# Kernel optimization log

Measured on AMD Instinct MI355X. Metric: run time of the kernel, lower is better.

## Reference

```python
import jax, jax.numpy as jnp
import numpy as np

N, E = 50000, 800000
IN, OUT = 128, 64  # in_channels, out_channels


def _w(key, fan_in, fan_out):
    return jax.random.normal(key, (fan_in, fan_out), dtype=jnp.float32) * (1.0 / np.sqrt(fan_in))


def setup_inputs() -> dict:
    key = jax.random.key(0)
    ks = jax.random.split(key, 16)
    x = jax.random.normal(ks[0], (N, IN), dtype=jnp.float32)
    edge_index = jax.random.randint(ks[1], (2, E), 0, N, dtype=jnp.int64)
    return {
        "x": x,
        "edge_index": edge_index,
        # Encoder: GCNConv(128->128), GCNConv(128->64), Linear(64->64)
        "ew1": _w(ks[2], IN, 2 * OUT), "eb1": jnp.zeros((2 * OUT,), jnp.float32),
        "ew2": _w(ks[3], 2 * OUT, OUT), "eb2": jnp.zeros((OUT,), jnp.float32),
        "efw": _w(ks[4], OUT, OUT), "efb": jnp.zeros((OUT,), jnp.float32),
        # Decoder: GCNConv(64->256), GCNConv(256->128), Linear(128->1024)
        "dw1": _w(ks[5], OUT, 2 * IN), "db1": jnp.zeros((2 * IN,), jnp.float32),
        "dw2": _w(ks[6], 2 * IN, IN), "db2": jnp.zeros((IN,), jnp.float32),
        "dfw": _w(ks[7], IN, 1024), "dfb": jnp.zeros((1024,), jnp.float32),
        # LinkPredictor: Linear(2*64 -> 1)
        "lw": _w(ks[8], 2 * OUT, 1), "lb": jnp.zeros((1,), jnp.float32),
    }


def gcn_conv(h_in, W, b, src, dst, dinv):
    # PyG GCNConv: linear transform, then symmetric-normalized aggregation
    # with implicit self-loops (deg includes the self-loop).
    h = h_in @ W  # [N, F_out]
    norm = (dinv[src] * dinv[dst])[:, None]      # per-edge symmetric norm
    agg = jax.ops.segment_sum(h[src] * norm, dst, num_segments=h.shape[0])
    agg = agg + h * (dinv * dinv)[:, None]       # self-loop contribution
    return agg + b


def reference(x, edge_index, ew1, eb1, ew2, eb2, efw, efb,
              dw1, db1, dw2, db2, dfw, dfb, lw, lb):
    src, dst = edge_index[0], edge_index[1]
    n = x.shape[0]
    # degree over A + I (self-loops added), computed on the target index
    deg = jax.ops.segment_sum(jnp.ones((src.shape[0],), x.dtype), dst,
                              num_segments=n) + 1.0
    dinv = deg ** -0.5

    # Encoder
    z = jax.nn.relu(gcn_conv(x, ew1, eb1, src, dst, dinv))
    z = gcn_conv(z, ew2, eb2, src, dst, dinv)
    z = z @ efw + efb  # latent [N, 64]

    # Decoder
    h = jax.nn.relu(gcn_conv(z, dw1, db1, src, dst, dinv))
    h = gcn_conv(h, dw2, db2, src, dst, dinv)
    x_hat = h @ dfw + dfb  # [N, 1024]

    # Link predictor on edge endpoint gathers
    zc = jnp.concatenate([z[src], z[dst]], axis=-1)  # [E, 128]
    edge_probs = jax.nn.sigmoid(zc @ lw + lb)        # [E, 1]
    return x_hat, edge_probs
```

## Files before the change

### kernel.cpp

```cpp
#include <hip/hip_runtime.h>
#include <hip/hip_bf16.h>

using bf16 = __hip_bfloat16;
typedef __attribute__((ext_vector_type(8))) short short8;
typedef __attribute__((ext_vector_type(4))) float f32x4;

static __device__ __forceinline__ float b2f(bf16 x) { return __bfloat162float(x); }

static __device__ __forceinline__ unsigned int packbf2(float a, float b) {
    bf16 x = __float2bfloat16(a), y = __float2bfloat16(b);
    unsigned short ux = *(unsigned short*)&x, uy = *(unsigned short*)&y;
    return (unsigned int)ux | ((unsigned int)uy << 16);
}

__global__ void det_kernel(const unsigned short* __restrict__ xh,
                           const int* __restrict__ ei, int* __restrict__ flags) {
    __shared__ int s_exp, s_nz;
    if (threadIdx.x == 0) { s_exp = 0; s_nz = 0; }
    __syncthreads();
    if (threadIdx.x < 256) {
        unsigned short h = xh[threadIdx.x];
        int ef = (h >> 7) & 0xFF;
        if (ef < 100 || ef > 140) atomicAdd(&s_exp, 1);
    }
    for (int i = 1 + 2 * threadIdx.x; i < 4096; i += 2 * blockDim.x)
        if (ei[i] != 0) atomicAdd(&s_nz, 1);
    __syncthreads();
    if (threadIdx.x == 0) {
        flags[0] = (s_exp > 16) ? 1 : 0;
        flags[1] = (s_nz == 0) ? 1 : 0;
    }
}

__global__ void canon_w(const void* __restrict__ src, const int* __restrict__ flags,
                        float* __restrict__ dst, int n) {
    int i = blockIdx.x * blockDim.x + threadIdx.x;
    if (i >= n) return;
    dst[i] = flags[0] ? ((const float*)src)[i] : b2f(((const bf16*)src)[i]);
}

__global__ void canon_x(const void* __restrict__ src, const int* __restrict__ flags,
                        bf16* __restrict__ dst, int n) {
    int i = blockIdx.x * blockDim.x + threadIdx.x;
    if (i >= n) return;
    dst[i] = flags[0] ? __float2bfloat16(((const float*)src)[i]) : ((const bf16*)src)[i];
}

__global__ void canon_edges(const int* __restrict__ ei, const int* __restrict__ flags,
                            int* __restrict__ srcd, int* __restrict__ dstd, int E) {
    int e = blockIdx.x * blockDim.x + threadIdx.x;
    if (e >= E) return;
    if (flags[1]) { srcd[e] = ei[2 * e]; dstd[e] = ei[2 * E + 2 * e]; }
    else          { srcd[e] = ei[e];     dstd[e] = ei[E + e]; }
}

__global__ void prep_wt(const void* __restrict__ src, const int* __restrict__ flags,
                        bf16* __restrict__ Wth, bf16* __restrict__ Wtl, int K, int F) {
    int j = blockIdx.x * blockDim.x + threadIdx.x;
    if (j >= K * F) return;
    int f = j / K, k = j - f * K;
    float v = flags[0] ? ((const float*)src)[(size_t)k * F + f]
                       : b2f(((const bf16*)src)[(size_t)k * F + f]);
    bf16 hi = __float2bfloat16(v);
    float lo = v - b2f(hi);
    Wth[j] = hi;
    Wtl[j] = __float2bfloat16(lo);
}

__global__ void hist_kernel(const int* __restrict__ dstv, int* __restrict__ counts, int E) {
    int e = blockIdx.x * blockDim.x + threadIdx.x;
    if (e < E) atomicAdd(&counts[dstv[e]], 1);
}

__global__ void scan_part1(const int* __restrict__ counts, int* __restrict__ blockSums, int N) {
    __shared__ int red[256];
    int i = blockIdx.x * 256 + threadIdx.x;
    red[threadIdx.x] = (i < N) ? counts[i] : 0;
    __syncthreads();
    for (int off = 128; off > 0; off >>= 1) {
        if (threadIdx.x < off) red[threadIdx.x] += red[threadIdx.x + off];
        __syncthreads();
    }
    if (threadIdx.x == 0) blockSums[blockIdx.x] = red[0];
}

__global__ void scan_part2(const int* __restrict__ blockSums, int* __restrict__ blockOff,
                           int* __restrict__ rowPtrN, int G) {
    __shared__ int s[256];
    int t = threadIdx.x;
    s[t] = (t < G) ? blockSums[t] : 0;
    __syncthreads();
    for (int off = 1; off < 256; off <<= 1) {
        int v = (t >= off) ? s[t - off] : 0;
        __syncthreads();
        s[t] += v;
        __syncthreads();
    }
    if (t < G) blockOff[t] = (t > 0) ? s[t - 1] : 0;
    if (t == 255) *rowPtrN = s[255];
}

__global__ void scan_part3(const int* __restrict__ counts, const int* __restrict__ blockOff,
                           int* __restrict__ rowPtr, int* __restrict__ cursor,
                           float* __restrict__ dinv, int N) {
    __shared__ int s[256];
    int t = threadIdx.x;
    int i = blockIdx.x * 256 + t;
    int c = (i < N) ? counts[i] : 0;
    s[t] = c;
    __syncthreads();
    for (int off = 1; off < 256; off <<= 1) {
        int v = (t >= off) ? s[t - off] : 0;
        __syncthreads();
        s[t] += v;
        __syncthreads();
    }
    if (i < N) {
        int o = blockOff[blockIdx.x] + s[t] - c;
        rowPtr[i] = o;
        cursor[i] = o;
        dinv[i] = rsqrtf((float)c + 1.0f);
    }
}

__global__ void scatter_kernel(const int* __restrict__ srcv, const int* __restrict__ dstv,
                               int* __restrict__ cursor, int* __restrict__ sortedSrc, int E) {
    int e = blockIdx.x * blockDim.x + threadIdx.x;
    if (e >= E) return;
    int p = atomicAdd(&cursor[dstv[e]], 1);
    sortedSrc[p] = srcv[e];
}

template <int K>
__global__ __launch_bounds__(256)
void mfma_gemm(const bf16* __restrict__ A,
               const bf16* __restrict__ Wth, const bf16* __restrict__ Wtl,
               const float* __restrict__ bias, const float* __restrict__ dinv,
               void* __restrict__ out, const int* __restrict__ flags,
               int outmode, int F, int N) {
    __shared__ uint4 lds4[1536];
    char* lds = (char*)lds4;
    const int tid = threadIdx.x;
    const int w = tid >> 6, lane = tid & 63;
    const int rowBase = blockIdx.y * 64;
    const int colBase = blockIdx.x * 64;

    f32x4 zero = {0.f, 0.f, 0.f, 0.f};
    f32x4 acc[4];
#pragma unroll
    for (int n = 0; n < 4; ++n) acc[n] = zero;

    const int arow = (w << 4) + (lane & 15);
    const int aswz = arow & 7;
    const int colL = lane & 15;

    for (int kc = 0; kc < K; kc += 64) {
#pragma unroll
        for (int i = 0; i < 6; ++i) {
            const int g = i * 256 + tid;
            char* dst = lds + ((i * 256 + (w << 6)) << 4);
            const bf16* src;
            if (g < 512) {
                int r = g >> 3, c = g & 7;
                int gr = rowBase + r; if (gr >= N) gr = N - 1;
                src = A + (size_t)gr * K + kc + ((c ^ (r & 7)) << 3);
            } else if (g < 1024) {
                int h = g - 512; int cl = h >> 3, c = h & 7;
                src = Wth + (size_t)(colBase + cl) * K + kc + ((c ^ (cl & 7)) << 3);
            } else {
                int h = g - 1024; int cl = h >> 3, c = h & 7;
                src = Wtl + (size_t)(colBase + cl) * K + kc + ((c ^ (cl & 7)) << 3);
            }
            __builtin_amdgcn_global_load_lds(
                (const __attribute__((address_space(1))) void*)src,
                (__attribute__((address_space(3))) void*)dst, 16, 0, 0);
        }
        __syncthreads();

        const char* aB = lds;
        const char* hB = lds + 8192;
        const char* lB = lds + 16384;
#pragma unroll
        for (int ks = 0; ks < 2; ++ks) {
            const int c = (ks << 2) + (lane >> 4);
            short8 a = *(const short8*)(aB + (((arow << 3) + (c ^ aswz)) << 4));
#pragma unroll
            for (int n = 0; n < 4; ++n) {
                const int col = (n << 4) + colL;
                const int s = ((col << 3) + (c ^ (col & 7))) << 4;
                short8 bh = *(const short8*)(hB + s);
                short8 bl = *(const short8*)(lB + s);
                acc[n] = __builtin_amdgcn_mfma_f32_16x16x32_bf16(a, bh, acc[n], 0, 0, 0);
                acc[n] = __builtin_amdgcn_mfma_f32_16x16x32_bf16(a, bl, acc[n], 0, 0, 0);
            }
        }
        __syncthreads();
    }

    const int m32 = outmode ? flags[0] : 0;
    const int r0 = rowBase + (w << 4) + ((lane >> 4) << 2);
#pragma unroll
    for (int n = 0; n < 4; ++n) {
        const int col = colBase + (n << 4) + colL;
        const float bv = bias ? bias[col] : 0.0f;
#pragma unroll
        for (int r = 0; r < 4; ++r) {
            const int row = r0 + r;
            if (row < N) {
                float v = acc[n][r];
                if (dinv) v *= dinv[row];
                v += bv;
                size_t o = (size_t)row * F + col;
                if (m32) ((float*)out)[o] = v;
                else     ((bf16*)out)[o] = __float2bfloat16(v);
            }
        }
    }
}

template <int F>
static __device__ __forceinline__ void acc_row(const bf16* __restrict__ Hs, int row, int lane,
                                               float* acc) {
    if constexpr (F == 64) {
        unsigned short u = ((const unsigned short*)Hs)[(size_t)row * 64 + lane];
        union { unsigned int i; float f; } c; c.i = (unsigned int)u << 16;
        acc[0] += c.f;
    } else if constexpr (F == 128) {
        unsigned int u = ((const unsigned int*)(Hs + (size_t)row * 128))[lane];
        union { unsigned int i; float f; } lo, hi;
        lo.i = u << 16; hi.i = u & 0xffff0000u;
        acc[0] += lo.f; acc[1] += hi.f;
    } else {
        uint2 u = ((const uint2*)(Hs + (size_t)row * 256))[lane];
        union { unsigned int i; float f; } a, b, c, d;
        a.i = u.x << 16; b.i = u.x & 0xffff0000u;
        c.i = u.y << 16; d.i = u.y & 0xffff0000u;
        acc[0] += a.f; acc[1] += b.f; acc[2] += c.f; acc[3] += d.f;
    }
}

template <int F>
__global__ void gather_kernel(const bf16* __restrict__ Hs, const int* __restrict__ rowPtr,
                              const int* __restrict__ sortedSrc, const float* __restrict__ dinv,
                              const float* __restrict__ bias, bf16* __restrict__ out,
                              int relu, int N) {
    constexpr int WPL = F / 64;
    int node = blockIdx.x * (blockDim.x >> 6) + (threadIdx.x >> 6);
    int lane = threadIdx.x & 63;
    if (node >= N) return;
    float acc[WPL];
#pragma unroll
    for (int w = 0; w < WPL; ++w) acc[w] = 0.0f;
    acc_row<F>(Hs, node, lane, acc);
    const int beg = rowPtr[node], end = rowPtr[node + 1];
    for (int b = beg; b < end; b += 64) {
        int n = end - b; if (n > 64) n = 64;
        int myS = (lane < n) ? sortedSrc[b + lane] : 0;
        int j = 0;
        for (; j + 1 < n; j += 2) {
            int s0 = __shfl(myS, j), s1 = __shfl(myS, j + 1);
            acc_row<F>(Hs, s0, lane, acc);
            acc_row<F>(Hs, s1, lane, acc);
        }
        if (j < n) acc_row<F>(Hs, __shfl(myS, j), lane, acc);
    }
    const float di = dinv[node];
    if constexpr (F == 64) {
        float v = acc[0] * di + bias[lane];
        if (relu) v = fmaxf(v, 0.0f);
        bf16 o = __float2bfloat16(v);
        ((unsigned short*)out)[(size_t)node * 64 + lane] = *(unsigned short*)&o;
    } else if constexpr (F == 128) {
        float v0 = acc[0] * di + bias[2 * lane];
        float v1 = acc[1] * di + bias[2 * lane + 1];
        if (relu) { v0 = fmaxf(v0, 0.0f); v1 = fmaxf(v1, 0.0f); }
        ((unsigned int*)(out + (size_t)node * 128))[lane] = packbf2(v0, v1);
    } else {
        float v0 = acc[0] * di + bias[4 * lane];
        float v1 = acc[1] * di + bias[4 * lane + 1];
        float v2 = acc[2] * di + bias[4 * lane + 2];
        float v3 = acc[3] * di + bias[4 * lane + 3];
        if (relu) { v0 = fmaxf(v0, 0.0f); v1 = fmaxf(v1, 0.0f);
                    v2 = fmaxf(v2, 0.0f); v3 = fmaxf(v3, 0.0f); }
        uint2 p; p.x = packbf2(v0, v1); p.y = packbf2(v2, v3);
        ((uint2*)(out + (size_t)node * 256))[lane] = p;
    }
}

__global__ void link_pre(const bf16* __restrict__ Z, const float* __restrict__ lw,
                         float* __restrict__ ab, int N) {
    int node = blockIdx.x * (blockDim.x >> 6) + (threadIdx.x >> 6);
    int lane = threadIdx.x & 63;
    if (node >= N) return;
    float zv = b2f(Z[(size_t)node * 64 + lane]);
    float va = zv * lw[lane];
    float vb = zv * lw[64 + lane];
#pragma unroll
    for (int off = 32; off > 0; off >>= 1) {
        va += __shfl_down(va, off);
        vb += __shfl_down(vb, off);
    }
    if (lane == 0) { ab[2 * node] = va; ab[2 * node + 1] = vb; }
}

__global__ void link_edge(const float* __restrict__ ab, const int* __restrict__ srcv,
                          const int* __restrict__ dstv, const float* __restrict__ lb,
                          void* __restrict__ out, const int* __restrict__ flags,
                          size_t outOff, int E) {
    int e = blockIdx.x * blockDim.x + threadIdx.x;
    if (e >= E) return;
    float v = ab[2 * srcv[e]] + ab[2 * dstv[e] + 1] + lb[0];
    float sv = 1.0f / (1.0f + expf(-v));
    if (flags[0]) ((float*)out)[outOff + e] = sv;
    else          ((bf16*)out)[outOff + e] = __float2bfloat16(sv);
}

extern "C" void kernel_launch(void* const* d_in, const int* in_sizes, int n_in,
                              void* d_out, int out_size, void* d_ws, size_t ws_size,
                              hipStream_t stream) {
    const int N = in_sizes[0] / 128;
    const int E = in_sizes[1] / 2;

    char* base = (char*)d_ws;
    size_t off = 0;
    auto alloc = [&](size_t bytes) { char* p = base + off; off = (off + bytes + 255) & ~(size_t)255; return p; };
    int*   flags  = (int*)  alloc(256);
    float* dinv   = (float*)alloc((size_t)N * 4);
    float* Wc     = (float*)alloc((size_t)210689 * 4);
    int*   counts = (int*)  alloc((size_t)N * 4);
    int*   rowPtr = (int*)  alloc(((size_t)N + 1) * 4);
    int*   cursor = (int*)  alloc((size_t)N * 4);
    int*   sortedSrc = (int*)alloc((size_t)E * 4);
    int*   srcd   = (int*)  alloc((size_t)E * 4);
    int*   dstd   = (int*)  alloc((size_t)E * 4);
    bf16*  Hs     = (bf16*) alloc((size_t)N * 256 * 2);
    bf16*  P0     = (bf16*) alloc((size_t)N * 256 * 2);
    bf16*  z      = (bf16*) alloc((size_t)N * 64 * 2);
    bf16*  Wth    = (bf16*) alloc((size_t)208896 * 2);
    bf16*  Wtl    = (bf16*) alloc((size_t)208896 * 2);
    float* ab     = (float*)alloc((size_t)N * 2 * 4);
    int*   blockSums = (int*)alloc(256 * 4);
    int*   blockOff  = (int*)alloc(256 * 4);

    const int W_EB1 = 16384, W_EB2 = 24704, W_EFB = 28864, W_DB1 = 45312,
              W_DB2 = 78336, W_DFB = 209536, W_LW = 210560, W_LB = 210688;
    const int T_EW1 = 0, T_EW2 = 16384, T_EFW = 24576, T_DW1 = 28672,
              T_DW2 = 45056, T_DFW = 77824;

    det_kernel<<<1, 256, 0, stream>>>((const unsigned short*)d_in[0], (const int*)d_in[1], flags);
    canon_edges<<<(E + 255) / 256, 256, 0, stream>>>((const int*)d_in[1], flags, srcd, dstd, E);

    hipMemsetAsync(counts, 0, (size_t)N * 4, stream);
    hist_kernel<<<(E + 255) / 256, 256, 0, stream>>>(dstd, counts, E);
    const int gScan = (N + 255) / 256;
    scan_part1<<<gScan, 256, 0, stream>>>(counts, blockSums, N);
    scan_part2<<<1, 256, 0, stream>>>(blockSums, blockOff, rowPtr + N, gScan);
    scan_part3<<<gScan, 256, 0, stream>>>(counts, blockOff, rowPtr, cursor, dinv, N);
    scatter_kernel<<<(E + 255) / 256, 256, 0, stream>>>(srcd, dstd, cursor, sortedSrc, E);

    {
        const int idx[8]  = {3, 5, 7, 9, 11, 13, 14, 15};
        const int woff[8] = {W_EB1, W_EB2, W_EFB, W_DB1, W_DB2, W_DFB, W_LW, W_LB};
        for (int j = 0; j < 8; ++j) {
            int n = in_sizes[idx[j]];
            canon_w<<<(n + 255) / 256, 256, 0, stream>>>(d_in[idx[j]], flags, Wc + woff[j], n);
        }
    }
    {
        const int idx[6]  = {2, 4, 6, 8, 10, 12};
        const int toff[6] = {T_EW1, T_EW2, T_EFW, T_DW1, T_DW2, T_DFW};
        const int kk[6]   = {128, 128, 64, 64, 256, 128};
        const int ff[6]   = {128, 64, 64, 256, 128, 1024};
        for (int j = 0; j < 6; ++j) {
            int n = kk[j] * ff[j];
            prep_wt<<<(n + 255) / 256, 256, 0, stream>>>(d_in[idx[j]], flags,
                                                         Wth + toff[j], Wtl + toff[j], kk[j], ff[j]);
        }
    }
    canon_x<<<(N * 128 + 255) / 256, 256, 0, stream>>>(d_in[0], flags, P0, N * 128);

    const int gRB = (N + 63) / 64;
    const int gG = (N + 3) / 4;

    mfma_gemm<128><<<dim3(2, gRB), 256, 0, stream>>>(P0, Wth + T_EW1, Wtl + T_EW1,
                                                     nullptr, dinv, Hs, flags, 0, 128, N);
    gather_kernel<128><<<gG, 256, 0, stream>>>(Hs, rowPtr, sortedSrc, dinv, Wc + W_EB1, P0, 1, N);

    mfma_gemm<128><<<dim3(1, gRB), 256, 0, stream>>>(P0, Wth + T_EW2, Wtl + T_EW2,
                                                     nullptr, dinv, Hs, flags, 0, 64, N);
    gather_kernel<64><<<gG, 256, 0, stream>>>(Hs, rowPtr, sortedSrc, dinv, Wc + W_EB2, P0, 0, N);

    mfma_gemm<64><<<dim3(1, gRB), 256, 0, stream>>>(P0, Wth + T_EFW, Wtl + T_EFW,
                                                    Wc + W_EFB, nullptr, z, flags, 0, 64, N);

    link_pre<<<gG, 256, 0, stream>>>(z, Wc + W_LW, ab, N);

    mfma_gemm<64><<<dim3(4, gRB), 256, 0, stream>>>(z, Wth + T_DW1, Wtl + T_DW1,
                                                    nullptr, dinv, Hs, flags, 0, 256, N);
    gather_kernel<256><<<gG, 256, 0, stream>>>(Hs, rowPtr, sortedSrc, dinv, Wc + W_DB1, P0, 1, N);

    mfma_gemm<256><<<dim3(2, gRB), 256, 0, stream>>>(P0, Wth + T_DW2, Wtl + T_DW2,
                                                     nullptr, dinv, Hs, flags, 0, 128, N);
    gather_kernel<128><<<gG, 256, 0, stream>>>(Hs, rowPtr, sortedSrc, dinv, Wc + W_DB2, P0, 0, N);

    mfma_gemm<128><<<dim3(16, gRB), 256, 0, stream>>>(P0, Wth + T_DFW, Wtl + T_DFW,
                                                      Wc + W_DFB, nullptr, d_out, flags, 1, 1024, N);

    link_edge<<<(E + 255) / 256, 256, 0, stream>>>(ab, srcd, dstd, Wc + W_LB,
                                                   d_out, flags, (size_t)N * 1024, E);
}
```

Before: 689.8 us.

## Aggregate before transform in decoder layer 1, batch prep launches, fuse edge hist

```diff
diff --git a/kernel.cpp b/kernel.cpp
--- a/kernel.cpp
+++ b/kernel.cpp
@@ -32,11 +32,16 @@
     }
 }
 
-__global__ void canon_w(const void* __restrict__ src, const int* __restrict__ flags,
-                        float* __restrict__ dst, int n) {
-    int i = blockIdx.x * blockDim.x + threadIdx.x;
-    if (i >= n) return;
-    dst[i] = flags[0] ? ((const float*)src)[i] : b2f(((const bf16*)src)[i]);
+struct CanonWB { const void* src[8]; float* dst[8]; int n[8]; };
+
+__global__ void canon_w_batch(CanonWB cb, const int* __restrict__ flags) {
+    int j = blockIdx.x;
+    const void* src = cb.src[j];
+    float* dst = cb.dst[j];
+    int n = cb.n[j];
+    int m32 = flags[0];
+    for (int i = threadIdx.x; i < n; i += blockDim.x)
+        dst[i] = m32 ? ((const float*)src)[i] : b2f(((const bf16*)src)[i]);
 }
 
 __global__ void canon_x(const void* __restrict__ src, const int* __restrict__ flags,
@@ -46,30 +51,38 @@
     dst[i] = flags[0] ? __float2bfloat16(((const float*)src)[i]) : ((const bf16*)src)[i];
 }
 
-__global__ void canon_edges(const int* __restrict__ ei, const int* __restrict__ flags,
-                            int* __restrict__ srcd, int* __restrict__ dstd, int E) {
+__global__ void canon_edges_hist(const int* __restrict__ ei, const int* __restrict__ flags,
+                                 int* __restrict__ srcd, int* __restrict__ dstd,
+                                 int* __restrict__ counts, int E) {
     int e = blockIdx.x * blockDim.x + threadIdx.x;
     if (e >= E) return;
-    if (flags[1]) { srcd[e] = ei[2 * e]; dstd[e] = ei[2 * E + 2 * e]; }
-    else          { srcd[e] = ei[e];     dstd[e] = ei[E + e]; }
-}
-
-__global__ void prep_wt(const void* __restrict__ src, const int* __restrict__ flags,
-                        bf16* __restrict__ Wth, bf16* __restrict__ Wtl, int K, int F) {
-    int j = blockIdx.x * blockDim.x + threadIdx.x;
-    if (j >= K * F) return;
-    int f = j / K, k = j - f * K;
-    float v = flags[0] ? ((const float*)src)[(size_t)k * F + f]
-                       : b2f(((const bf16*)src)[(size_t)k * F + f]);
+    int s, d;
+    if (flags[1]) { s = ei[2 * e]; d = ei[2 * E + 2 * e]; }
+    else          { s = ei[e];     d = ei[E + e]; }
+    srcd[e] = s; dstd[e] = d;
+    atomicAdd(&counts[d], 1);
+}
+
+struct PrepB { const void* src[6]; int lgK[6]; int F[6]; int off[6]; int end[6]; };
+
+__global__ void prep_wt_batch(PrepB pb, const int* __restrict__ flags,
+                              bf16* __restrict__ Wth, bf16* __restrict__ Wtl, int total) {
+    int g = blockIdx.x * blockDim.x + threadIdx.x;
+    if (g >= total) return;
+    int j = 0;
+#pragma unroll
+    for (int t = 0; t < 6; ++t) if (g >= pb.end[t]) j = t + 1;
+    const void* src = pb.src[j];
+    int lgK = pb.lgK[j], F = pb.F[j];
+    int local = g - pb.off[j];
+    int f = local >> lgK, k = local & ((1 << lgK) - 1);
+    float v = flags[0] ? ((const float*)src)[((size_t)k << 0) * F + (size_t)k * (F - 1) ? 0 : 0] : 0.0f;
+    v = flags[0] ? ((const float*)src)[(size_t)k * F + f]
+                 : b2f(((const bf16*)src)[(size_t)k * F + f]);
     bf16 hi = __float2bfloat16(v);
     float lo = v - b2f(hi);
-    Wth[j] = hi;
-    Wtl[j] = __float2bfloat16(lo);
-}
-
-__global__ void hist_kernel(const int* __restrict__ dstv, int* __restrict__ counts, int E) {
-    int e = blockIdx.x * blockDim.x + threadIdx.x;
-    if (e < E) atomicAdd(&counts[dstv[e]], 1);
+    Wth[g] = hi;
+    Wtl[g] = __float2bfloat16(lo);
 }
 
 __global__ void scan_part1(const int* __restrict__ counts, int* __restrict__ blockSums, int N) {
@@ -137,7 +150,8 @@
                const bf16* __restrict__ Wth, const bf16* __restrict__ Wtl,
                const float* __restrict__ bias, const float* __restrict__ dinv,
                void* __restrict__ out, const int* __restrict__ flags,
-               int outmode, int F, int N) {
+               int outmode, int relu, bf16* __restrict__ out2,
+               const float* __restrict__ dinv2, int F, int N) {
     __shared__ uint4 lds4[1536];
     char* lds = (char*)lds4;
     const int tid = threadIdx.x;
@@ -210,9 +224,11 @@
                 float v = acc[n][r];
                 if (dinv) v *= dinv[row];
                 v += bv;
+                if (relu) v = fmaxf(v, 0.0f);
                 size_t o = (size_t)row * F + col;
                 if (m32) ((float*)out)[o] = v;
                 else     ((bf16*)out)[o] = __float2bfloat16(v);
+                if (out2) out2[o] = __float2bfloat16(v * dinv2[row]);
             }
         }
     }
@@ -257,29 +273,33 @@
         int n = end - b; if (n > 64) n = 64;
         int myS = (lane < n) ? sortedSrc[b + lane] : 0;
         int j = 0;
-        for (; j + 1 < n; j += 2) {
-            int s0 = __shfl(myS, j), s1 = __shfl(myS, j + 1);
+        for (; j + 3 < n; j += 4) {
+            int s0 = __shfl(myS, j),     s1 = __shfl(myS, j + 1);
+            int s2 = __shfl(myS, j + 2), s3 = __shfl(myS, j + 3);
             acc_row<F>(Hs, s0, lane, acc);
             acc_row<F>(Hs, s1, lane, acc);
-        }
-        if (j < n) acc_row<F>(Hs, __shfl(myS, j), lane, acc);
+            acc_row<F>(Hs, s2, lane, acc);
+            acc_row<F>(Hs, s3, lane, acc);
+        }
+        for (; j < n; ++j) acc_row<F>(Hs, __shfl(myS, j), lane, acc);
     }
     const float di = dinv[node];
     if constexpr (F == 64) {
-        float v = acc[0] * di + bias[lane];
+        float v = acc[0] * di + (bias ? bias[lane] : 0.0f);
         if (relu) v = fmaxf(v, 0.0f);
         bf16 o = __float2bfloat16(v);
         ((unsigned short*)out)[(size_t)node * 64 + lane] = *(unsigned short*)&o;
     } else if constexpr (F == 128) {
-        float v0 = acc[0] * di + bias[2 * lane];
-        float v1 = acc[1] * di + bias[2 * lane + 1];
+        float b0 = bias ? bias[2 * lane] : 0.0f, b1 = bias ? bias[2 * lane + 1] : 0.0f;
+        float v0 = acc[0] * di + b0;
+        float v1 = acc[1] * di + b1;
         if (relu) { v0 = fmaxf(v0, 0.0f); v1 = fmaxf(v1, 0.0f); }
         ((unsigned int*)(out + (size_t)node * 128))[lane] = packbf2(v0, v1);
     } else {
-        float v0 = acc[0] * di + bias[4 * lane];
-        float v1 = acc[1] * di + bias[4 * lane + 1];
-        float v2 = acc[2] * di + bias[4 * lane + 2];
-        float v3 = acc[3] * di + bias[4 * lane + 3];
+        float v0 = acc[0] * di + (bias ? bias[4 * lane] : 0.0f);
+        float v1 = acc[1] * di + (bias ? bias[4 * lane + 1] : 0.0f);
+        float v2 = acc[2] * di + (bias ? bias[4 * lane + 2] : 0.0f);
+        float v3 = acc[3] * di + (bias ? bias[4 * lane + 3] : 0.0f);
         if (relu) { v0 = fmaxf(v0, 0.0f); v1 = fmaxf(v1, 0.0f);
                     v2 = fmaxf(v2, 0.0f); v3 = fmaxf(v3, 0.0f); }
         uint2 p; p.x = packbf2(v0, v1); p.y = packbf2(v2, v3);
@@ -336,6 +356,7 @@
     bf16*  Hs     = (bf16*) alloc((size_t)N * 256 * 2);
     bf16*  P0     = (bf16*) alloc((size_t)N * 256 * 2);
     bf16*  z      = (bf16*) alloc((size_t)N * 64 * 2);
+    bf16*  zs     = (bf16*) alloc((size_t)N * 64 * 2);
     bf16*  Wth    = (bf16*) alloc((size_t)208896 * 2);
     bf16*  Wtl    = (bf16*) alloc((size_t)208896 * 2);
     float* ab     = (float*)alloc((size_t)N * 2 * 4);
@@ -348,10 +369,10 @@
               T_DW2 = 45056, T_DFW = 77824;
 
     det_kernel<<<1, 256, 0, stream>>>((const unsigned short*)d_in[0], (const int*)d_in[1], flags);
-    canon_edges<<<(E + 255) / 256, 256, 0, stream>>>((const int*)d_in[1], flags, srcd, dstd, E);
 
     hipMemsetAsync(counts, 0, (size_t)N * 4, stream);
-    hist_kernel<<<(E + 255) / 256, 256, 0, stream>>>(dstd, counts, E);
+    canon_edges_hist<<<(E + 255) / 256, 256, 0, stream>>>((const int*)d_in[1], flags,
+                                                          srcd, dstd, counts, E);
     const int gScan = (N + 255) / 256;
     scan_part1<<<gScan, 256, 0, stream>>>(counts, blockSums, N);
     scan_part2<<<1, 256, 0, stream>>>(blockSums, blockOff, rowPtr + N, gScan);
@@ -359,23 +380,32 @@
     scatter_kernel<<<(E + 255) / 256, 256, 0, stream>>>(srcd, dstd, cursor, sortedSrc, E);
 
     {
+        CanonWB cb;
         const int idx[8]  = {3, 5, 7, 9, 11, 13, 14, 15};
         const int woff[8] = {W_EB1, W_EB2, W_EFB, W_DB1, W_DB2, W_DFB, W_LW, W_LB};
         for (int j = 0; j < 8; ++j) {
-            int n = in_sizes[idx[j]];
-            canon_w<<<(n + 255) / 256, 256, 0, stream>>>(d_in[idx[j]], flags, Wc + woff[j], n);
-        }
+            cb.src[j] = d_in[idx[j]];
+            cb.dst[j] = Wc + woff[j];
+            cb.n[j] = in_sizes[idx[j]];
+        }
+        canon_w_batch<<<8, 256, 0, stream>>>(cb, flags);
     }
     {
+        PrepB pb;
         const int idx[6]  = {2, 4, 6, 8, 10, 12};
         const int toff[6] = {T_EW1, T_EW2, T_EFW, T_DW1, T_DW2, T_DFW};
-        const int kk[6]   = {128, 128, 64, 64, 256, 128};
+        const int lgk[6]  = {7, 7, 6, 6, 8, 7};
         const int ff[6]   = {128, 64, 64, 256, 128, 1024};
+        int total = 0;
         for (int j = 0; j < 6; ++j) {
-            int n = kk[j] * ff[j];
-            prep_wt<<<(n + 255) / 256, 256, 0, stream>>>(d_in[idx[j]], flags,
-                                                         Wth + toff[j], Wtl + toff[j], kk[j], ff[j]);
-        }
+            pb.src[j] = d_in[idx[j]];
+            pb.lgK[j] = lgk[j];
+            pb.F[j] = ff[j];
+            pb.off[j] = toff[j];
+            pb.end[j] = toff[j] + (ff[j] << lgk[j]);
+            total = pb.end[j];
+        }
+        prep_wt_batch<<<(total + 255) / 256, 256, 0, stream>>>(pb, flags, Wth, Wtl, total);
     }
     canon_x<<<(N * 128 + 255) / 256, 256, 0, stream>>>(d_in[0], flags, P0, N * 128);
 
@@ -383,28 +413,34 @@
     const int gG = (N + 3) / 4;
 
     mfma_gemm<128><<<dim3(2, gRB), 256, 0, stream>>>(P0, Wth + T_EW1, Wtl + T_EW1,
-                                                     nullptr, dinv, Hs, flags, 0, 128, N);
+                                                     nullptr, dinv, Hs, flags, 0, 0,
+                                                     nullptr, nullptr, 128, N);
     gather_kernel<128><<<gG, 256, 0, stream>>>(Hs, rowPtr, sortedSrc, dinv, Wc + W_EB1, P0, 1, N);
 
     mfma_gemm<128><<<dim3(1, gRB), 256, 0, stream>>>(P0, Wth + T_EW2, Wtl + T_EW2,
-                                                     nullptr, dinv, Hs, flags, 0, 64, N);
+                                                     nullptr, dinv, Hs, flags, 0, 0,
+                                                     nullptr, nullptr, 64, N);
     gather_kernel<64><<<gG, 256, 0, stream>>>(Hs, rowPtr, sortedSrc, dinv, Wc + W_EB2, P0, 0, N);
 
     mfma_gemm<64><<<dim3(1, gRB), 256, 0, stream>>>(P0, Wth + T_EFW, Wtl + T_EFW,
-                                                    Wc + W_EFB, nullptr, z, flags, 0, 64, N);
+                                                    Wc + W_EFB, nullptr, z, flags, 0, 0,
+                                                    zs, dinv, 64, N);
 
     link_pre<<<gG, 256, 0, stream>>>(z, Wc + W_LW, ab, N);
 
-    mfma_gemm<64><<<dim3(4, gRB), 256, 0, stream>>>(z, Wth + T_DW1, Wtl + T_DW1,
-                                                    nullptr, dinv, Hs, flags, 0, 256, N);
-    gather_kernel<256><<<gG, 256, 0, stream>>>(Hs, rowPtr, sortedSrc, dinv, Wc + W_DB1, P0, 1, N);
+    gather_kernel<64><<<gG, 256, 0, stream>>>(zs, rowPtr, sortedSrc, dinv, nullptr, Hs, 0, N);
+    mfma_gemm<64><<<dim3(4, gRB), 256, 0, stream>>>(Hs, Wth + T_DW1, Wtl + T_DW1,
+                                                    Wc + W_DB1, nullptr, P0, flags, 0, 1,
+                                                    nullptr, nullptr, 256, N);
 
     mfma_gemm<256><<<dim3(2, gRB), 256, 0, stream>>>(P0, Wth + T_DW2, Wtl + T_DW2,
-                                                     nullptr, dinv, Hs, flags, 0, 128, N);
+                                                     nullptr, dinv, Hs, flags, 0, 0,
+                                                     nullptr, nullptr, 128, N);
     gather_kernel<128><<<gG, 256, 0, stream>>>(Hs, rowPtr, sortedSrc, dinv, Wc + W_DB2, P0, 0, N);
 
     mfma_gemm<128><<<dim3(16, gRB), 256, 0, stream>>>(P0, Wth + T_DFW, Wtl + T_DFW,
-                                                      Wc + W_DFB, nullptr, d_out, flags, 1, 1024, N);
+                                                      Wc + W_DFB, nullptr, d_out, flags, 1, 0,
+                                                      nullptr, nullptr, 1024, N);
 
     link_edge<<<(E + 255) / 256, 256, 0, stream>>>(ab, srcd, dstd, Wc + W_LB,
                                                    d_out, flags, (size_t)N * 1024, E);
```

Result: faster. 621.3 us (-9.9%).
